# Kernel tuning notes

Hardware: AMD Instinct MI355X
Metric: run time of the kernel (lower is better)

Reference implementation:

```python
import jax, jax.numpy as jnp
import numpy as np

SIGMA = 2.0  # gaussian decay std, matches test_cfg.sigma default


def setup_inputs() -> dict:
    key = jax.random.key(0)
    k1, k2, k3 = jax.random.split(key, 3)
    N, H, W = 200, 400, 608
    masks = jax.random.uniform(k1, (N, H, W), dtype=jnp.float32)
    scores = jax.random.uniform(k2, (N,), dtype=jnp.float32)
    labels = jax.random.randint(k3, (N,), 0, 80)
    return {"masks": masks, "scores": scores, "labels": labels}


def reference(masks, scores, labels):
    # Matrix NMS (SOLOv2): sort by score, IoU via one big matmul, triu mask,
    # per-class gaussian decay, rescale scores, re-sort.
    N = masks.shape[0]
    mask_area = masks.sum((1, 2))  # (N,)

    order = jnp.argsort(-scores)  # descending sort indices
    scores_s = scores[order]
    masks_s = masks[order]
    area_s = mask_area[order]
    labels_s = labels[order]

    flat = masks_s.reshape(N, -1)              # (N, H*W)
    inter = flat @ flat.T                       # (N, N) intersection
    iou = inter / (area_s[:, None] + area_s[None, :] - inter)
    triu = jnp.triu(jnp.ones((N, N), dtype=bool), 1)
    label_match = (labels_s[:, None] == labels_s[None, :]) & triu
    decay_iou = jnp.where(label_match, iou, 0.0)  # iou.triu(1) * label_matrix

    compensate = decay_iou.max(0)               # (N,) max IoU over higher-scored same-class
    decay_matrix = jnp.exp(-SIGMA * decay_iou ** 2)
    compensate_matrix = jnp.exp(-SIGMA * compensate[:, None] ** 2)
    decay_coef = (decay_matrix / compensate_matrix).min(0)  # (N,)

    new_scores = scores_s * decay_coef
    order2 = jnp.argsort(-new_scores)
    keep_inds = order[order2]
    return (new_scores[order2], labels_s[order2], masks_s[order2], keep_inds)
```

## Files before the change

### kernel.cpp

```cpp
#include <hip/hip_runtime.h>
#include <stdint.h>

#define N_DET 200
#define HW 243200
#define NP 208
#define NT 13
#define KSTEPS 3800
#define GS 256
#define SPB 15
#define TRI_TILES 91
#define PART_STRIDE (TRI_TILES * 256)
#define LDS_STRIDE 72
#define HWV (HW / 4)
#define GATHER_VECS (N_DET * HWV)

typedef __attribute__((ext_vector_type(8))) short bf16x8v;
typedef __attribute__((ext_vector_type(4))) float f32x4;

__device__ __forceinline__ unsigned short f32_to_bf16(float f) {
    union { float f; uint32_t i; } v; v.f = f;
    uint32_t lsb = (v.i >> 16) & 1u;
    v.i += 0x7FFFu + lsb;
    return (unsigned short)(v.i >> 16);
}

__device__ __forceinline__ void pack8(const float4& a, const float4& b, uint4& out) {
    unsigned short u[8];
    u[0] = f32_to_bf16(a.x); u[1] = f32_to_bf16(a.y);
    u[2] = f32_to_bf16(a.z); u[3] = f32_to_bf16(a.w);
    u[4] = f32_to_bf16(b.x); u[5] = f32_to_bf16(b.y);
    u[6] = f32_to_bf16(b.z); u[7] = f32_to_bf16(b.w);
    out = *(const uint4*)u;
}

__global__ __launch_bounds__(832) void gram_kernel(const float* __restrict__ masks,
                                                   float* __restrict__ partial) {
    __shared__ unsigned short lds[2][NP * LDS_STRIDE];
    const int kb = blockIdx.x;
    const int s0 = kb * SPB;
    const int s1 = min(KSTEPS, s0 + SPB);

    f32x4 acc[NT];
#pragma unroll
    for (int j = 0; j < NT; ++j) acc[j] = (f32x4){0.f, 0.f, 0.f, 0.f};

    const int t = threadIdx.x;
    const int lane = t & 63, wv = t >> 6;
    const int frow = lane & 15;
    const int koff = (lane >> 4) * 8;
    const int srow = t >> 3;
    const int scol = (t & 7) * 8;

    const int r0 = srow, r1 = srow + 104;
    const float* src0 = masks + (size_t)r0 * HW + scol;
    const float* src1 = masks + (size_t)r1 * HW + scol;

    float4 f0a, f0b, f1a, f1b;

    if (s0 < s1) {
        const int k0 = s0 * 64;
        if (r0 < N_DET) { f0a = *(const float4*)(src0 + k0); f0b = *(const float4*)(src0 + k0 + 4); }
        if (r1 < N_DET) { f1a = *(const float4*)(src1 + k0); f1b = *(const float4*)(src1 + k0 + 4); }
        uint4 w0, w1;
        if (r0 < N_DET) pack8(f0a, f0b, w0);
        else { const unsigned short fl = (r0 == N_DET) ? 0x3F80 : 0; unsigned short u[8];
#pragma unroll
               for (int i = 0; i < 8; ++i) u[i] = fl; w0 = *(const uint4*)u; }
        if (r1 < N_DET) pack8(f1a, f1b, w1);
        else { const unsigned short fl = (r1 == N_DET) ? 0x3F80 : 0; unsigned short u[8];
#pragma unroll
               for (int i = 0; i < 8; ++i) u[i] = fl; w1 = *(const uint4*)u; }
        *(uint4*)&lds[0][r0 * LDS_STRIDE + scol] = w0;
        *(uint4*)&lds[0][r1 * LDS_STRIDE + scol] = w1;
        __syncthreads();

        int cur = 0;
        for (int s = s0; s < s1; ++s) {
            const bool has_next = (s + 1 < s1);
            if (has_next) {
                const int kn = (s + 1) * 64;
                if (r0 < N_DET) { f0a = *(const float4*)(src0 + kn); f0b = *(const float4*)(src0 + kn + 4); }
                if (r1 < N_DET) { f1a = *(const float4*)(src1 + kn); f1b = *(const float4*)(src1 + kn + 4); }
            }

            const unsigned short* bp = &lds[cur][0];
            bf16x8v a0 = *(const bf16x8v*)&bp[(wv * 16 + frow) * LDS_STRIDE + koff];
            bf16x8v a1 = *(const bf16x8v*)&bp[(wv * 16 + frow) * LDS_STRIDE + 32 + koff];
#pragma unroll
            for (int jt = 0; jt < NT; ++jt) {
                if (jt < wv) continue;
                bf16x8v b0, b1;
                if (jt == wv) { b0 = a0; b1 = a1; }
                else {
                    b0 = *(const bf16x8v*)&bp[(jt * 16 + frow) * LDS_STRIDE + koff];
                    b1 = *(const bf16x8v*)&bp[(jt * 16 + frow) * LDS_STRIDE + 32 + koff];
                }
                acc[jt] = __builtin_amdgcn_mfma_f32_16x16x32_bf16(a0, b0, acc[jt], 0, 0, 0);
                acc[jt] = __builtin_amdgcn_mfma_f32_16x16x32_bf16(a1, b1, acc[jt], 0, 0, 0);
            }

            if (has_next) {
                uint4 w0, w1;
                if (r0 < N_DET) pack8(f0a, f0b, w0);
                else { const unsigned short fl = (r0 == N_DET) ? 0x3F80 : 0; unsigned short u[8];
#pragma unroll
                       for (int i = 0; i < 8; ++i) u[i] = fl; w0 = *(const uint4*)u; }
                if (r1 < N_DET) pack8(f1a, f1b, w1);
                else { const unsigned short fl = (r1 == N_DET) ? 0x3F80 : 0; unsigned short u[8];
#pragma unroll
                       for (int i = 0; i < 8; ++i) u[i] = fl; w1 = *(const uint4*)u; }
                *(uint4*)&lds[cur ^ 1][r0 * LDS_STRIDE + scol] = w0;
                *(uint4*)&lds[cur ^ 1][r1 * LDS_STRIDE + scol] = w1;
            }
            __syncthreads();
            cur ^= 1;
        }
    }

    float* pp = partial + (size_t)kb * PART_STRIDE;
    const int tbase = wv * 13 - (wv * (wv - 1)) / 2 - wv;
    const int row16 = (lane >> 4) * 4;
    const int col16 = lane & 15;
#pragma unroll
    for (int jt = 0; jt < NT; ++jt) {
        if (jt < wv) continue;
        const int tile = tbase + jt;
#pragma unroll
        for (int r = 0; r < 4; ++r)
            pp[tile * 256 + (row16 + r) * 16 + col16] = acc[jt][r];
    }
}

__global__ void reduce_kernel(const float* __restrict__ partial,
                              float* __restrict__ gram) {
    const int tr = blockIdx.x, tc = blockIdx.y;
    if (tc < tr) return;
    const int tile = tr * 13 - (tr * (tr - 1)) / 2 + (tc - tr);
    const int idx = threadIdx.x;
    const float* p = partial + tile * 256 + idx;
    float s = 0.f;
#pragma unroll 32
    for (int g = 0; g < GS; ++g) s += p[(size_t)g * PART_STRIDE];
    const int r = tr * 16 + (idx >> 4);
    const int c = tc * 16 + (idx & 15);
    gram[r * NP + c] = s;
    if (tr != tc) gram[c * NP + r] = s;
}

__global__ __launch_bounds__(1024) void nms_kernel(const float* __restrict__ scores_in,
                                                   const int* __restrict__ labels,
                                                   const float* __restrict__ gram,
                                                   float* __restrict__ out_scores,
                                                   float* __restrict__ out_labels,
                                                   float* __restrict__ out_keep) {
    __shared__ float sc[N_DET];
    __shared__ int   lab[N_DET];
    __shared__ float ar[N_DET];
    __shared__ int   order_[N_DET];
    __shared__ float sc_s[N_DET];
    __shared__ int   lab_s[N_DET];
    __shared__ float ar_s[N_DET];
    __shared__ float comp[N_DET];
    __shared__ float part[N_DET][4];
    __shared__ float nsc[N_DET];
    __shared__ int   ord2[N_DET];

    const int t = threadIdx.x;
    if (t < N_DET) {
        sc[t]  = scores_in[t];
        lab[t] = labels[t];
        ar[t]  = gram[N_DET * NP + t];
    }
    __syncthreads();

    if (t < N_DET) {
        const float si = sc[t];
        int r = 0;
        for (int j = 0; j < N_DET; ++j) {
            const float sj = sc[j];
            if (sj > si || (sj == si && j < t)) ++r;
        }
        order_[r] = t;
    }
    __syncthreads();
    if (t < N_DET) { const int o = order_[t]; sc_s[t] = sc[o]; lab_s[t] = lab[o]; ar_s[t] = ar[o]; }
    __syncthreads();

    const int j = t >> 2, sub = t & 3;
    if (j < N_DET) {
        float m = 0.f;
        const int oj = order_[j];
        const float aj = ar_s[j];
        const int lj = lab_s[j];
        for (int i = sub; i < j; i += 4) {
            if (lab_s[i] == lj) {
                const float g = gram[order_[i] * NP + oj];
                const float iou = g / (ar_s[i] + aj - g);
                m = fmaxf(m, iou);
            }
        }
        part[j][sub] = m;
    }
    __syncthreads();
    if (t < N_DET) comp[t] = fmaxf(fmaxf(part[t][0], part[t][1]), fmaxf(part[t][2], part[t][3]));
    __syncthreads();

    if (j < N_DET) {
        float mn = 1e30f;
        const int oj = order_[j];
        const float aj = ar_s[j];
        const int lj = lab_s[j];
        for (int i = sub; i < N_DET; i += 4) {
            float d = 0.f;
            if (i < j && lab_s[i] == lj) {
                const float g = gram[order_[i] * NP + oj];
                d = g / (ar_s[i] + aj - g);
            }
            const float c = comp[i];
            const float val = expf(-2.0f * (d * d - c * c));
            mn = fminf(mn, val);
        }
        part[j][sub] = mn;
    }
    __syncthreads();
    if (t < N_DET) {
        const float mn = fminf(fminf(part[t][0], part[t][1]), fminf(part[t][2], part[t][3]));
        nsc[t] = sc_s[t] * mn;
    }
    __syncthreads();

    if (t < N_DET) {
        const float si = nsc[t];
        int r = 0;
        for (int k = 0; k < N_DET; ++k) {
            const float sk = nsc[k];
            if (sk > si || (sk == si && k < t)) ++r;
        }
        ord2[r] = t;
    }
    __syncthreads();

    if (t < N_DET) {
        const int jj = ord2[t];
        out_scores[t] = nsc[jj];
        out_labels[t] = (float)lab_s[jj];
        out_keep[t]   = (float)order_[jj];
    }
}

__global__ void gather_kernel(const float4* __restrict__ masks,
                              const float* __restrict__ keep,
                              float4* __restrict__ out_masks) {
    const int stride = gridDim.x * blockDim.x;
    for (int i = blockIdx.x * blockDim.x + threadIdx.x; i < GATHER_VECS; i += stride) {
        const int r = i / HWV;
        const int c = i - r * HWV;
        const int src = (int)keep[r];
        out_masks[i] = masks[(size_t)src * HWV + c];
    }
}

extern "C" void kernel_launch(void* const* d_in, const int* in_sizes, int n_in,
                              void* d_out, int out_size, void* d_ws, size_t ws_size,
                              hipStream_t stream) {
    const float* masks  = (const float*)d_in[0];
    const float* scores = (const float*)d_in[1];
    const int*   labels = (const int*)d_in[2];
    float* out = (float*)d_out;

    float* out_scores = out;
    float* out_labels = out + N_DET;
    float* out_masks  = out + 2 * N_DET;
    float* out_keep   = out + 2 * N_DET + (size_t)N_DET * HW;

    float* partial = out_masks;
    float* gram    = out_masks + (size_t)GS * PART_STRIDE;

    gram_kernel<<<GS, 832, 0, stream>>>(masks, partial);
    reduce_kernel<<<dim3(13, 13), 256, 0, stream>>>(partial, gram);
    nms_kernel<<<1, 1024, 0, stream>>>(scores, labels, gram,
                                       out_scores, out_labels, out_keep);
    gather_kernel<<<2048, 256, 0, stream>>>((const float4*)masks, out_keep, (float4*)out_masks);
}
```

Baseline: 152.1 us.

## Fuse gram, reduce, NMS and gather into one persistent kernel with grid barriers

Replaces the four separate kernel launches with a single persistent kernel of 256 blocks that uses atomic-counter grid barriers between phases: Gram matmul, partial reduction, single-block NMS, then mask gather. The intent is to remove the launch gaps and tail idle time between stages. The NMS rank computations are spread over 4 threads per element, and the gather uses nontemporal stores. In exchange, all blocks must be co-resident for the spin barrier to be safe, every block waits while block 0 runs the serial NMS phase, and an extra memset launch is added to reset the barrier counter.

```diff
diff --git a/kernel.cpp b/kernel.cpp
--- a/kernel.cpp
+++ b/kernel.cpp
@@ -13,6 +13,8 @@
 #define LDS_STRIDE 72
 #define HWV (HW / 4)
 #define GATHER_VECS (N_DET * HWV)
+#define NBLK 256
+#define NTHR 832
 
 typedef __attribute__((ext_vector_type(8))) short bf16x8v;
 typedef __attribute__((ext_vector_type(4))) float f32x4;
@@ -24,239 +26,274 @@
     return (unsigned short)(v.i >> 16);
 }
 
-__device__ __forceinline__ void pack8(const float4& a, const float4& b, uint4& out) {
+__device__ __forceinline__ uint4 pack8(const float4& a, const float4& b) {
     unsigned short u[8];
     u[0] = f32_to_bf16(a.x); u[1] = f32_to_bf16(a.y);
     u[2] = f32_to_bf16(a.z); u[3] = f32_to_bf16(a.w);
     u[4] = f32_to_bf16(b.x); u[5] = f32_to_bf16(b.y);
     u[6] = f32_to_bf16(b.z); u[7] = f32_to_bf16(b.w);
-    out = *(const uint4*)u;
-}
-
-__global__ __launch_bounds__(832) void gram_kernel(const float* __restrict__ masks,
-                                                   float* __restrict__ partial) {
-    __shared__ unsigned short lds[2][NP * LDS_STRIDE];
-    const int kb = blockIdx.x;
-    const int s0 = kb * SPB;
-    const int s1 = min(KSTEPS, s0 + SPB);
-
-    f32x4 acc[NT];
-#pragma unroll
-    for (int j = 0; j < NT; ++j) acc[j] = (f32x4){0.f, 0.f, 0.f, 0.f};
-
+    return *(const uint4*)u;
+}
+
+struct NmsS {
+    float sc[N_DET];   int lab[N_DET];   float ar[N_DET];
+    int   order_[N_DET]; float sc_s[N_DET]; int lab_s[N_DET]; float ar_s[N_DET];
+    float comp[N_DET]; float part[N_DET][4]; int ipart[N_DET][4];
+    float nsc[N_DET];  int ord2[N_DET];
+};
+union SmemU {
+    unsigned short gram[2][NP * LDS_STRIDE];
+    NmsS nms;
+};
+
+__device__ __forceinline__ void grid_barrier(unsigned* bar, int use) {
+    __syncthreads();
+    if (threadIdx.x == 0) {
+        __threadfence();
+        __hip_atomic_fetch_add(bar, 1u, __ATOMIC_RELEASE, __HIP_MEMORY_SCOPE_AGENT);
+        const unsigned target = (unsigned)NBLK * (unsigned)(use + 1);
+        while (__hip_atomic_load(bar, __ATOMIC_ACQUIRE, __HIP_MEMORY_SCOPE_AGENT) < target)
+            __builtin_amdgcn_s_sleep(8);
+        __threadfence();
+    }
+    __syncthreads();
+}
+
+__global__ __launch_bounds__(NTHR) void mega_kernel(const float* __restrict__ masks,
+                                                    const float* __restrict__ scores_in,
+                                                    const int* __restrict__ labels,
+                                                    float* __restrict__ out_scores,
+                                                    float* __restrict__ out_labels,
+                                                    float* __restrict__ out_masks,
+                                                    float* __restrict__ out_keep,
+                                                    float* __restrict__ partial,
+                                                    float* __restrict__ gram,
+                                                    unsigned* __restrict__ bar) {
+    __shared__ SmemU smem;
     const int t = threadIdx.x;
-    const int lane = t & 63, wv = t >> 6;
-    const int frow = lane & 15;
-    const int koff = (lane >> 4) * 8;
-    const int srow = t >> 3;
-    const int scol = (t & 7) * 8;
-
-    const int r0 = srow, r1 = srow + 104;
-    const float* src0 = masks + (size_t)r0 * HW + scol;
-    const float* src1 = masks + (size_t)r1 * HW + scol;
-
-    float4 f0a, f0b, f1a, f1b;
-
-    if (s0 < s1) {
-        const int k0 = s0 * 64;
-        if (r0 < N_DET) { f0a = *(const float4*)(src0 + k0); f0b = *(const float4*)(src0 + k0 + 4); }
-        if (r1 < N_DET) { f1a = *(const float4*)(src1 + k0); f1b = *(const float4*)(src1 + k0 + 4); }
-        uint4 w0, w1;
-        if (r0 < N_DET) pack8(f0a, f0b, w0);
-        else { const unsigned short fl = (r0 == N_DET) ? 0x3F80 : 0; unsigned short u[8];
-#pragma unroll
-               for (int i = 0; i < 8; ++i) u[i] = fl; w0 = *(const uint4*)u; }
-        if (r1 < N_DET) pack8(f1a, f1b, w1);
-        else { const unsigned short fl = (r1 == N_DET) ? 0x3F80 : 0; unsigned short u[8];
-#pragma unroll
-               for (int i = 0; i < 8; ++i) u[i] = fl; w1 = *(const uint4*)u; }
-        *(uint4*)&lds[0][r0 * LDS_STRIDE + scol] = w0;
-        *(uint4*)&lds[0][r1 * LDS_STRIDE + scol] = w1;
-        __syncthreads();
-
-        int cur = 0;
-        for (int s = s0; s < s1; ++s) {
-            const bool has_next = (s + 1 < s1);
-            if (has_next) {
-                const int kn = (s + 1) * 64;
-                if (r0 < N_DET) { f0a = *(const float4*)(src0 + kn); f0b = *(const float4*)(src0 + kn + 4); }
-                if (r1 < N_DET) { f1a = *(const float4*)(src1 + kn); f1b = *(const float4*)(src1 + kn + 4); }
-            }
-
-            const unsigned short* bp = &lds[cur][0];
-            bf16x8v a0 = *(const bf16x8v*)&bp[(wv * 16 + frow) * LDS_STRIDE + koff];
-            bf16x8v a1 = *(const bf16x8v*)&bp[(wv * 16 + frow) * LDS_STRIDE + 32 + koff];
-#pragma unroll
-            for (int jt = 0; jt < NT; ++jt) {
-                if (jt < wv) continue;
-                bf16x8v b0, b1;
-                if (jt == wv) { b0 = a0; b1 = a1; }
-                else {
-                    b0 = *(const bf16x8v*)&bp[(jt * 16 + frow) * LDS_STRIDE + koff];
-                    b1 = *(const bf16x8v*)&bp[(jt * 16 + frow) * LDS_STRIDE + 32 + koff];
-                }
-                acc[jt] = __builtin_amdgcn_mfma_f32_16x16x32_bf16(a0, b0, acc[jt], 0, 0, 0);
-                acc[jt] = __builtin_amdgcn_mfma_f32_16x16x32_bf16(a1, b1, acc[jt], 0, 0, 0);
-            }
-
-            if (has_next) {
-                uint4 w0, w1;
-                if (r0 < N_DET) pack8(f0a, f0b, w0);
-                else { const unsigned short fl = (r0 == N_DET) ? 0x3F80 : 0; unsigned short u[8];
-#pragma unroll
-                       for (int i = 0; i < 8; ++i) u[i] = fl; w0 = *(const uint4*)u; }
-                if (r1 < N_DET) pack8(f1a, f1b, w1);
-                else { const unsigned short fl = (r1 == N_DET) ? 0x3F80 : 0; unsigned short u[8];
-#pragma unroll
-                       for (int i = 0; i < 8; ++i) u[i] = fl; w1 = *(const uint4*)u; }
-                *(uint4*)&lds[cur ^ 1][r0 * LDS_STRIDE + scol] = w0;
-                *(uint4*)&lds[cur ^ 1][r1 * LDS_STRIDE + scol] = w1;
-            }
+
+    {
+        const int kb = blockIdx.x;
+        const int s0 = kb * SPB;
+        const int s1 = min(KSTEPS, s0 + SPB);
+
+        f32x4 acc[NT];
+#pragma unroll
+        for (int j = 0; j < NT; ++j) acc[j] = (f32x4){0.f, 0.f, 0.f, 0.f};
+
+        const int lane = t & 63, wv = t >> 6;
+        const int frow = lane & 15;
+        const int koff = (lane >> 4) * 8;
+        const int srow = t >> 3;
+        const int scol = (t & 7) * 8;
+
+        const int r0 = srow, r1 = srow + 104;
+        const float* src0 = masks + (size_t)r0 * HW + scol;
+        const float* src1 = masks + (size_t)r1 * HW + scol;
+
+        float4 f0a, f0b, f1a, f1b;
+
+        if (s0 < s1) {
+            const int k0 = s0 * 64;
+            if (r0 < N_DET) { f0a = *(const float4*)(src0 + k0); f0b = *(const float4*)(src0 + k0 + 4); }
+            if (r1 < N_DET) { f1a = *(const float4*)(src1 + k0); f1b = *(const float4*)(src1 + k0 + 4); }
+            uint4 w0, w1;
+            if (r0 < N_DET) w0 = pack8(f0a, f0b);
+            else { const unsigned short fl = (r0 == N_DET) ? 0x3F80 : 0; unsigned short u[8];
+#pragma unroll
+                   for (int i = 0; i < 8; ++i) u[i] = fl; w0 = *(const uint4*)u; }
+            if (r1 < N_DET) w1 = pack8(f1a, f1b);
+            else { const unsigned short fl = (r1 == N_DET) ? 0x3F80 : 0; unsigned short u[8];
+#pragma unroll
+                   for (int i = 0; i < 8; ++i) u[i] = fl; w1 = *(const uint4*)u; }
+            *(uint4*)&smem.gram[0][r0 * LDS_STRIDE + scol] = w0;
+            *(uint4*)&smem.gram[0][r1 * LDS_STRIDE + scol] = w1;
             __syncthreads();
-            cur ^= 1;
-        }
-    }
-
-    float* pp = partial + (size_t)kb * PART_STRIDE;
-    const int tbase = wv * 13 - (wv * (wv - 1)) / 2 - wv;
-    const int row16 = (lane >> 4) * 4;
-    const int col16 = lane & 15;
-#pragma unroll
-    for (int jt = 0; jt < NT; ++jt) {
-        if (jt < wv) continue;
-        const int tile = tbase + jt;
-#pragma unroll
-        for (int r = 0; r < 4; ++r)
-            pp[tile * 256 + (row16 + r) * 16 + col16] = acc[jt][r];
-    }
-}
-
-__global__ void reduce_kernel(const float* __restrict__ partial,
-                              float* __restrict__ gram) {
-    const int tr = blockIdx.x, tc = blockIdx.y;
-    if (tc < tr) return;
-    const int tile = tr * 13 - (tr * (tr - 1)) / 2 + (tc - tr);
-    const int idx = threadIdx.x;
-    const float* p = partial + tile * 256 + idx;
-    float s = 0.f;
+
+            int cur = 0;
+            for (int s = s0; s < s1; ++s) {
+                const bool has_next = (s + 1 < s1);
+                if (has_next) {
+                    const int kn = (s + 1) * 64;
+                    if (r0 < N_DET) { f0a = *(const float4*)(src0 + kn); f0b = *(const float4*)(src0 + kn + 4); }
+                    if (r1 < N_DET) { f1a = *(const float4*)(src1 + kn); f1b = *(const float4*)(src1 + kn + 4); }
+                }
+
+                const unsigned short* bp = &smem.gram[cur][0];
+                bf16x8v a0 = *(const bf16x8v*)&bp[(wv * 16 + frow) * LDS_STRIDE + koff];
+                bf16x8v a1 = *(const bf16x8v*)&bp[(wv * 16 + frow) * LDS_STRIDE + 32 + koff];
+#pragma unroll
+                for (int jt = 0; jt < NT; ++jt) {
+                    if (jt < wv) continue;
+                    bf16x8v b0, b1;
+                    if (jt == wv) { b0 = a0; b1 = a1; }
+                    else {
+                        b0 = *(const bf16x8v*)&bp[(jt * 16 + frow) * LDS_STRIDE + koff];
+                        b1 = *(const bf16x8v*)&bp[(jt * 16 + frow) * LDS_STRIDE + 32 + koff];
+                    }
+                    acc[jt] = __builtin_amdgcn_mfma_f32_16x16x32_bf16(a0, b0, acc[jt], 0, 0, 0);
+                    acc[jt] = __builtin_amdgcn_mfma_f32_16x16x32_bf16(a1, b1, acc[jt], 0, 0, 0);
+                }
+
+                if (has_next) {
+                    uint4 w0n, w1n;
+                    if (r0 < N_DET) w0n = pack8(f0a, f0b);
+                    else { const unsigned short fl = (r0 == N_DET) ? 0x3F80 : 0; unsigned short u[8];
+#pragma unroll
+                           for (int i = 0; i < 8; ++i) u[i] = fl; w0n = *(const uint4*)u; }
+                    if (r1 < N_DET) w1n = pack8(f1a, f1b);
+                    else { const unsigned short fl = (r1 == N_DET) ? 0x3F80 : 0; unsigned short u[8];
+#pragma unroll
+                           for (int i = 0; i < 8; ++i) u[i] = fl; w1n = *(const uint4*)u; }
+                    *(uint4*)&smem.gram[cur ^ 1][r0 * LDS_STRIDE + scol] = w0n;
+                    *(uint4*)&smem.gram[cur ^ 1][r1 * LDS_STRIDE + scol] = w1n;
+                }
+                __syncthreads();
+                cur ^= 1;
+            }
+        }
+
+        float* pp = partial + (size_t)kb * PART_STRIDE;
+        const int tbase = wv * 13 - (wv * (wv - 1)) / 2 - wv;
+        const int row16 = (lane >> 4) * 4;
+        const int col16 = lane & 15;
+#pragma unroll
+        for (int jt = 0; jt < NT; ++jt) {
+            if (jt < wv) continue;
+            const int tile = tbase + jt;
+#pragma unroll
+            for (int r = 0; r < 4; ++r)
+                pp[tile * 256 + (row16 + r) * 16 + col16] = acc[jt][r];
+        }
+    }
+
+    grid_barrier(bar, 0);
+
+    if (blockIdx.x < TRI_TILES && t < 256) {
+        int tau = blockIdx.x, tr = 0;
+        while (tau >= NT - tr) { tau -= NT - tr; ++tr; }
+        const int tc = tr + tau;
+        const float* p = partial + blockIdx.x * 256 + t;
+        float s = 0.f;
 #pragma unroll 32
-    for (int g = 0; g < GS; ++g) s += p[(size_t)g * PART_STRIDE];
-    const int r = tr * 16 + (idx >> 4);
-    const int c = tc * 16 + (idx & 15);
-    gram[r * NP + c] = s;
-    if (tr != tc) gram[c * NP + r] = s;
-}
-
-__global__ __launch_bounds__(1024) void nms_kernel(const float* __restrict__ scores_in,
-                                                   const int* __restrict__ labels,
-                                                   const float* __restrict__ gram,
-                                                   float* __restrict__ out_scores,
-                                                   float* __restrict__ out_labels,
-                                                   float* __restrict__ out_keep) {
-    __shared__ float sc[N_DET];
-    __shared__ int   lab[N_DET];
-    __shared__ float ar[N_DET];
-    __shared__ int   order_[N_DET];
-    __shared__ float sc_s[N_DET];
-    __shared__ int   lab_s[N_DET];
-    __shared__ float ar_s[N_DET];
-    __shared__ float comp[N_DET];
-    __shared__ float part[N_DET][4];
-    __shared__ float nsc[N_DET];
-    __shared__ int   ord2[N_DET];
-
-    const int t = threadIdx.x;
-    if (t < N_DET) {
-        sc[t]  = scores_in[t];
-        lab[t] = labels[t];
-        ar[t]  = gram[N_DET * NP + t];
-    }
-    __syncthreads();
-
-    if (t < N_DET) {
-        const float si = sc[t];
-        int r = 0;
-        for (int j = 0; j < N_DET; ++j) {
-            const float sj = sc[j];
-            if (sj > si || (sj == si && j < t)) ++r;
-        }
-        order_[r] = t;
-    }
-    __syncthreads();
-    if (t < N_DET) { const int o = order_[t]; sc_s[t] = sc[o]; lab_s[t] = lab[o]; ar_s[t] = ar[o]; }
-    __syncthreads();
-
-    const int j = t >> 2, sub = t & 3;
-    if (j < N_DET) {
-        float m = 0.f;
-        const int oj = order_[j];
-        const float aj = ar_s[j];
-        const int lj = lab_s[j];
-        for (int i = sub; i < j; i += 4) {
-            if (lab_s[i] == lj) {
-                const float g = gram[order_[i] * NP + oj];
-                const float iou = g / (ar_s[i] + aj - g);
-                m = fmaxf(m, iou);
-            }
-        }
-        part[j][sub] = m;
-    }
-    __syncthreads();
-    if (t < N_DET) comp[t] = fmaxf(fmaxf(part[t][0], part[t][1]), fmaxf(part[t][2], part[t][3]));
-    __syncthreads();
-
-    if (j < N_DET) {
-        float mn = 1e30f;
-        const int oj = order_[j];
-        const float aj = ar_s[j];
-        const int lj = lab_s[j];
-        for (int i = sub; i < N_DET; i += 4) {
-            float d = 0.f;
-            if (i < j && lab_s[i] == lj) {
-                const float g = gram[order_[i] * NP + oj];
-                d = g / (ar_s[i] + aj - g);
-            }
-            const float c = comp[i];
-            const float val = expf(-2.0f * (d * d - c * c));
-            mn = fminf(mn, val);
-        }
-        part[j][sub] = mn;
-    }
-    __syncthreads();
-    if (t < N_DET) {
-        const float mn = fminf(fminf(part[t][0], part[t][1]), fminf(part[t][2], part[t][3]));
-        nsc[t] = sc_s[t] * mn;
-    }
-    __syncthreads();
-
-    if (t < N_DET) {
-        const float si = nsc[t];
-        int r = 0;
-        for (int k = 0; k < N_DET; ++k) {
-            const float sk = nsc[k];
-            if (sk > si || (sk == si && k < t)) ++r;
-        }
-        ord2[r] = t;
-    }
-    __syncthreads();
-
-    if (t < N_DET) {
-        const int jj = ord2[t];
-        out_scores[t] = nsc[jj];
-        out_labels[t] = (float)lab_s[jj];
-        out_keep[t]   = (float)order_[jj];
-    }
-}
-
-__global__ void gather_kernel(const float4* __restrict__ masks,
-                              const float* __restrict__ keep,
-                              float4* __restrict__ out_masks) {
-    const int stride = gridDim.x * blockDim.x;
-    for (int i = blockIdx.x * blockDim.x + threadIdx.x; i < GATHER_VECS; i += stride) {
-        const int r = i / HWV;
-        const int c = i - r * HWV;
-        const int src = (int)keep[r];
-        out_masks[i] = masks[(size_t)src * HWV + c];
+        for (int g = 0; g < GS; ++g) s += p[(size_t)g * PART_STRIDE];
+        const int r = tr * 16 + (t >> 4);
+        const int c = tc * 16 + (t & 15);
+        gram[r * NP + c] = s;
+        if (tr != tc) gram[c * NP + r] = s;
+    }
+
+    grid_barrier(bar, 1);
+
+    if (blockIdx.x == 0) {
+        NmsS& S = smem.nms;
+        const int i4 = t >> 2, s4 = t & 3;
+
+        if (t < N_DET) {
+            S.sc[t]  = scores_in[t];
+            S.lab[t] = labels[t];
+            S.ar[t]  = gram[N_DET * NP + t];
+        }
+        __syncthreads();
+
+        if (t < 800) {
+            const float si = S.sc[i4];
+            int r = 0;
+            for (int j = s4; j < N_DET; j += 4) {
+                const float sj = S.sc[j];
+                if (sj > si || (sj == si && j < i4)) ++r;
+            }
+            S.ipart[i4][s4] = r;
+        }
+        __syncthreads();
+        if (t < N_DET) {
+            const int r = S.ipart[t][0] + S.ipart[t][1] + S.ipart[t][2] + S.ipart[t][3];
+            S.order_[r] = t;
+        }
+        __syncthreads();
+        if (t < N_DET) { const int o = S.order_[t]; S.sc_s[t] = S.sc[o]; S.lab_s[t] = S.lab[o]; S.ar_s[t] = S.ar[o]; }
+        __syncthreads();
+
+        if (t < 800) {
+            float m = 0.f;
+            const int oj = S.order_[i4];
+            const float aj = S.ar_s[i4];
+            const int lj = S.lab_s[i4];
+            for (int i = s4; i < i4; i += 4) {
+                if (S.lab_s[i] == lj) {
+                    const float g = gram[S.order_[i] * NP + oj];
+                    const float iou = g / (S.ar_s[i] + aj - g);
+                    m = fmaxf(m, iou);
+                }
+            }
+            S.part[i4][s4] = m;
+        }
+        __syncthreads();
+        if (t < N_DET)
+            S.comp[t] = fmaxf(fmaxf(S.part[t][0], S.part[t][1]), fmaxf(S.part[t][2], S.part[t][3]));
+        __syncthreads();
+
+        if (t < 800) {
+            float mn = 1e30f;
+            const int oj = S.order_[i4];
+            const float aj = S.ar_s[i4];
+            const int lj = S.lab_s[i4];
+            for (int i = s4; i < N_DET; i += 4) {
+                float d = 0.f;
+                if (i < i4 && S.lab_s[i] == lj) {
+                    const float g = gram[S.order_[i] * NP + oj];
+                    d = g / (S.ar_s[i] + aj - g);
+                }
+                const float c = S.comp[i];
+                const float val = expf(-2.0f * (d * d - c * c));
+                mn = fminf(mn, val);
+            }
+            S.part[i4][s4] = mn;
+        }
+        __syncthreads();
+        if (t < N_DET) {
+            const float mn = fminf(fminf(S.part[t][0], S.part[t][1]), fminf(S.part[t][2], S.part[t][3]));
+            S.nsc[t] = S.sc_s[t] * mn;
+        }
+        __syncthreads();
+
+        if (t < 800) {
+            const float si = S.nsc[i4];
+            int r = 0;
+            for (int k = s4; k < N_DET; k += 4) {
+                const float sk = S.nsc[k];
+                if (sk > si || (sk == si && k < i4)) ++r;
+            }
+            S.ipart[i4][s4] = r;
+        }
+        __syncthreads();
+        if (t < N_DET) {
+            const int r = S.ipart[t][0] + S.ipart[t][1] + S.ipart[t][2] + S.ipart[t][3];
+            S.ord2[r] = t;
+        }
+        __syncthreads();
+
+        if (t < N_DET) {
+            const int jj = S.ord2[t];
+            out_scores[t] = S.nsc[jj];
+            out_labels[t] = (float)S.lab_s[jj];
+            out_keep[t]   = (float)S.order_[jj];
+        }
+    }
+
+    grid_barrier(bar, 2);
+
+    {
+        const f32x4* msk = (const f32x4*)masks;
+        f32x4* om = (f32x4*)out_masks;
+        const int stride = NBLK * NTHR;
+        for (int i = blockIdx.x * NTHR + t; i < GATHER_VECS; i += stride) {
+            const int r = i / HWV;
+            const int c = i - r * HWV;
+            const int src = (int)out_keep[r];
+            const f32x4 v = msk[(size_t)src * HWV + c];
+            __builtin_nontemporal_store(v, &om[i]);
+        }
     }
 }
 
@@ -275,10 +312,10 @@
 
     float* partial = out_masks;
     float* gram    = out_masks + (size_t)GS * PART_STRIDE;
-
-    gram_kernel<<<GS, 832, 0, stream>>>(masks, partial);
-    reduce_kernel<<<dim3(13, 13), 256, 0, stream>>>(partial, gram);
-    nms_kernel<<<1, 1024, 0, stream>>>(scores, labels, gram,
-                                       out_scores, out_labels, out_keep);
-    gather_kernel<<<2048, 256, 0, stream>>>((const float4*)masks, out_keep, (float4*)out_masks);
-}
+    unsigned* bar  = (unsigned*)d_ws;
+
+    hipMemsetAsync(bar, 0, 64, stream);
+    mega_kernel<<<NBLK, NTHR, 0, stream>>>(masks, scores, labels,
+                                           out_scores, out_labels, out_masks, out_keep,
+                                           partial, gram, bar);
+}
```

Result: slower. 285.4 us (+87.7%).
